# Performance work log

Measured on AMD Instinct MI355X. Metric: run time of the kernel, lower is better.

Reference implementation:

```python
import jax, jax.numpy as jnp
import numpy as np

N_NODES = 100000
IN_DIM = 128
HID = 128
N_EDGES = 1600000
N_PAIRS = 500000


def setup_inputs() -> dict:
    key = jax.random.key(0)
    ks = jax.random.split(key, 16)

    def lin(k, fan_out, fan_in):
        s = 1.0 / np.sqrt(fan_in)
        kw, kb = jax.random.split(k)
        W = jax.random.uniform(kw, (fan_out, fan_in), jnp.float32, -s, s)
        b = jax.random.uniform(kb, (fan_out,), jnp.float32, -s, s)
        return W, b

    x = jax.random.normal(ks[0], (N_NODES, IN_DIM), jnp.float32)
    edge_index = jax.random.randint(ks[1], (2, N_EDGES), 0, N_NODES, jnp.int64)
    edge_pairs = jax.random.randint(ks[2], (N_PAIRS, 2), 0, N_NODES, jnp.int64)

    # SAGEConv 1: lin_l (neighbor aggr, with bias), lin_r (root, no bias)
    W1l, b1l = lin(ks[3], HID, IN_DIM)
    W1r, _ = lin(ks[4], HID, IN_DIM)
    # SAGEConv 2
    W2l, b2l = lin(ks[5], HID, HID)
    W2r, _ = lin(ks[6], HID, HID)
    # MLP decoder
    Wm1, bm1 = lin(ks[7], HID, HID)
    Wm2, bm2 = lin(ks[8], HID // 2, HID)
    Wm3, bm3 = lin(ks[9], 1, HID // 2)

    return dict(x=x, edge_index=edge_index, edge_pairs=edge_pairs,
                W1l=W1l, b1l=b1l, W1r=W1r,
                W2l=W2l, b2l=b2l, W2r=W2r,
                Wm1=Wm1, bm1=bm1, Wm2=Wm2, bm2=bm2, Wm3=Wm3, bm3=bm3)


def _sage_conv(x, src, dst, Wl, bl, Wr):
    # mean aggregation of source-node features into destination nodes
    msg_sum = jax.ops.segment_sum(x[src], dst, num_segments=N_NODES)  # [N, D]
    cnt = jax.ops.segment_sum(jnp.ones((src.shape[0],), x.dtype), dst,
                              num_segments=N_NODES)
    aggr = msg_sum / jnp.maximum(cnt, 1.0)[:, None]
    return aggr @ Wl.T + bl + x @ Wr.T


def reference(x, edge_index, edge_pairs,
              W1l, b1l, W1r, W2l, b2l, W2r,
              Wm1, bm1, Wm2, bm2, Wm3, bm3):
    src, dst = edge_index[0], edge_index[1]
    # encode (eval mode: dropout = identity)
    h = jax.nn.relu(_sage_conv(x, src, dst, W1l, b1l, W1r))
    z = _sage_conv(h, src, dst, W2l, b2l, W2r)  # [N, HID]
    # decode
    hp = z[edge_pairs[:, 0]] * z[edge_pairs[:, 1]]  # [P, HID]
    hp = jax.nn.relu(hp @ Wm1.T + bm1)
    hp = jax.nn.relu(hp @ Wm2.T + bm2)
    return (hp @ Wm3.T + bm3).squeeze(-1)  # [P]
```

## Files before the change

kernel.cpp:

```cpp
#include <hip/hip_runtime.h>
#include <stdint.h>

typedef _Float16 half8 __attribute__((ext_vector_type(8)));
typedef float float4v __attribute__((ext_vector_type(4)));
typedef float floatx4 __attribute__((ext_vector_type(4)));
typedef int intx2 __attribute__((ext_vector_type(2)));

constexpr int kN = 100000;
constexpr int kE = 1600000;
constexpr int kP = 500000;
constexpr int NBS = (kN + 255) / 256;
constexpr int CT3 = kN / 16;
constexpr int DT2 = kP / 32;

__global__ void prep_kernel(
    const int* __restrict__ dst, int* __restrict__ deg, int* __restrict__ slot,
    const float* __restrict__ x, _Float16* __restrict__ xh,
    const float* __restrict__ W1l, const float* __restrict__ W1r,
    const float* __restrict__ W2l, const float* __restrict__ W2r,
    const float* __restrict__ Wm1, const float* __restrict__ Wm2,
    _Float16* __restrict__ CW1h, _Float16* __restrict__ CW1e,
    _Float16* __restrict__ CW2h, _Float16* __restrict__ CW2e,
    _Float16* __restrict__ M1h,  _Float16* __restrict__ M2h)
{
    const int b = blockIdx.x;
    if (b < 6250) {
        const int e = b * 256 + threadIdx.x;
        if (e < kE) slot[e] = atomicAdd(&deg[dst[e]], 1);
    } else if (b < 12500) {
        const int i = ((b - 6250) * 256 + threadIdx.x) * 8;
        if (i >= kN * 128) return;
        const floatx4 a = __builtin_nontemporal_load((const floatx4*)&x[i]);
        const floatx4 bb = __builtin_nontemporal_load((const floatx4*)&x[i + 4]);
        half8 v;
        v[0] = (_Float16)a[0]; v[1] = (_Float16)a[1]; v[2] = (_Float16)a[2]; v[3] = (_Float16)a[3];
        v[4] = (_Float16)bb[0]; v[5] = (_Float16)bb[1]; v[6] = (_Float16)bb[2]; v[7] = (_Float16)bb[3];
        *(half8*)&xh[i] = v;
    } else {
        const int i = (b - 12500) * 256 + threadIdx.x;
        if (i < 32768) {
            const int o = i >> 8, k = i & 255;
            const float w = (k < 128) ? W1l[o * 128 + k] : W1r[o * 128 + k - 128];
            const _Float16 h = (_Float16)w;
            CW1h[i] = h; CW1e[i] = (_Float16)(w - (float)h);
        } else if (i < 65536) {
            const int j = i - 32768;
            const int o = j >> 8, k = j & 255;
            const float w = (k < 128) ? W2l[o * 128 + k] : W2r[o * 128 + k - 128];
            const _Float16 h = (_Float16)w;
            CW2h[j] = h; CW2e[j] = (_Float16)(w - (float)h);
        } else if (i < 81920) {
            const int j = i - 65536;
            M1h[j] = (_Float16)Wm1[j];
        } else if (i < 90112) {
            const int j = i - 81920;
            M2h[j] = (_Float16)Wm2[j];
        }
    }
}

__global__ void scan_block_sums(const int* __restrict__ deg, int* __restrict__ bsum) {
    __shared__ int red[256];
    int t = threadIdx.x;
    int i = blockIdx.x * 256 + t;
    red[t] = (i < kN) ? deg[i] : 0;
    __syncthreads();
    for (int s = 128; s > 0; s >>= 1) {
        if (t < s) red[t] += red[t + s];
        __syncthreads();
    }
    if (t == 0) bsum[blockIdx.x] = red[0];
}

__global__ void scan_bsums(const int* __restrict__ bsum, int* __restrict__ boff) {
    __shared__ int sm[512];
    int t = threadIdx.x;
    int orig = (t < NBS) ? bsum[t] : 0;
    sm[t] = orig;
    __syncthreads();
    for (int d = 1; d < 512; d <<= 1) {
        int u = (t >= d) ? sm[t - d] : 0;
        __syncthreads();
        sm[t] += u;
        __syncthreads();
    }
    if (t < NBS) boff[t] = sm[t] - orig;
}

__global__ void scan_write(const int* __restrict__ deg, const int* __restrict__ boff,
                           int* __restrict__ row_start) {
    __shared__ int sm[256];
    int t = threadIdx.x;
    int i = blockIdx.x * 256 + t;
    int v = (i < kN) ? deg[i] : 0;
    sm[t] = v;
    __syncthreads();
    for (int d = 1; d < 256; d <<= 1) {
        int u = (t >= d) ? sm[t - d] : 0;
        __syncthreads();
        sm[t] += u;
        __syncthreads();
    }
    int excl = sm[t] - v + boff[blockIdx.x];
    if (i < kN) row_start[i] = excl;
    if (i == kN - 1) row_start[kN] = excl + v;
}

__global__ void fill2_kernel(const int* __restrict__ src, const int* __restrict__ dst,
                             const int* __restrict__ row_start,
                             const int* __restrict__ slot, int* __restrict__ srcs) {
    int e = blockIdx.x * blockDim.x + threadIdx.x;
    if (e < kE) srcs[row_start[dst[e]] + slot[e]] = src[e];
}

template <bool RELU>
__global__ __launch_bounds__(64, 4) void conv_mfma(
    const _Float16* __restrict__ xin,
    const int* __restrict__ row_start,
    const int* __restrict__ srcs,
    const _Float16* __restrict__ Wh,
    const _Float16* __restrict__ We,
    const float* __restrict__ bias,
    _Float16* __restrict__ out)
{
    __shared__ __align__(16) _Float16 stg[16 * 136];
    const int l = threadIdx.x & 63;
    const int p = l & 15;
    const int q = l >> 4;
    const int tile = blockIdx.x;
    const int c = p * 8;
    const int lbase = l & 48;

    int j0[4], j1[4];
#pragma unroll
    for (int s = 0; s < 4; s++) {
        const int n = tile * 16 + s * 4 + q;
        j0[s] = row_start[n];
        j1[s] = row_start[n + 1];
    }
    int idx16[4];
#pragma unroll
    for (int s = 0; s < 4; s++) {
        const int tA = j0[s] + p;
        const int v  = __builtin_nontemporal_load(&srcs[tA]);
        idx16[s] = (tA < j1[s]) ? v : 0;
    }

#pragma unroll
    for (int s = 0; s < 4; s++) {
        const int cnt = j1[s] - j0[s];
        float facc[8];
#pragma unroll
        for (int u = 0; u < 8; u++) facc[u] = 0.f;

        for (int jc = j0[s]; jc < j1[s]; jc += 16) {
            int myidx;
            if (jc == j0[s]) {
                myidx = idx16[s];
            } else {
                const int tB = jc + p;
                const int v  = __builtin_nontemporal_load(&srcs[tB]);
                myidx = (tB < j1[s]) ? v : 0;
            }
            half8 rows[16];
#pragma unroll
            for (int i = 0; i < 16; i++) {
                const int sidx = __shfl(myidx, lbase + i);
                rows[i] = *(const half8*)&xin[(size_t)sidx * 128 + c];
            }
            __builtin_amdgcn_sched_barrier(0);
            const int rem = j1[s] - jc;
#pragma unroll
            for (int i = 0; i < 16; i++) {
                if (i < rem) {
#pragma unroll
                    for (int u = 0; u < 8; u++) facc[u] += (float)rows[i][u];
                }
            }
        }
        const float inv = 1.0f / (float)(cnt > 1 ? cnt : 1);
        half8 hv;
#pragma unroll
        for (int u = 0; u < 8; u++) hv[u] = (_Float16)(facc[u] * inv);
        *(half8*)&stg[(s * 4 + q) * 136 + c] = hv;
    }

    half8 rt[4];
#pragma unroll
    for (int kt = 0; kt < 4; kt++)
        rt[kt] = *(const half8*)&xin[(size_t)(tile * 16 + p) * 128 + kt * 32 + q * 8];

    half8 am[4];
#pragma unroll
    for (int kt = 0; kt < 4; kt++)
        am[kt] = *(const half8*)&stg[p * 136 + kt * 32 + q * 8];

    float4v acc[8];
#pragma unroll
    for (int nt = 0; nt < 8; nt++) {
        const float b = bias[nt * 16 + p];
        acc[nt][0] = b; acc[nt][1] = b; acc[nt][2] = b; acc[nt][3] = b;
    }
#pragma unroll
    for (int kt = 0; kt < 8; kt++) {
        const half8 a = (kt < 4) ? am[kt] : rt[kt - 4];
#pragma unroll
        for (int nt = 0; nt < 8; nt++) {
            const int widx = (nt * 16 + p) * 256 + kt * 32 + q * 8;
            const half8 bh = *(const half8*)&Wh[widx];
            const half8 be = *(const half8*)&We[widx];
            acc[nt] = __builtin_amdgcn_mfma_f32_16x16x32_f16(a, bh, acc[nt], 0, 0, 0);
            acc[nt] = __builtin_amdgcn_mfma_f32_16x16x32_f16(a, be, acc[nt], 0, 0, 0);
        }
    }

#pragma unroll
    for (int nt = 0; nt < 8; nt++)
#pragma unroll
        for (int r = 0; r < 4; r++) {
            float v = acc[nt][r];
            if (RELU) v = fmaxf(v, 0.f);
            stg[(q * 4 + r) * 136 + nt * 16 + p] = (_Float16)v;
        }
    {
        const int row = l >> 2;
        const int c2  = (l & 3) * 8;
#pragma unroll
        for (int i = 0; i < 4; i++) {
            const half8 v = *(const half8*)&stg[row * 136 + i * 32 + c2];
            __builtin_nontemporal_store(v,
                (half8*)&out[(size_t)(tile * 16 + row) * 128 + i * 32 + c2]);
        }
    }
}

__global__ __launch_bounds__(64, 4) void decoder_mfma(
    const _Float16* __restrict__ z,
    const int* __restrict__ pairs,
    const _Float16* __restrict__ M1h, const float* __restrict__ bm1,
    const _Float16* __restrict__ M2h, const float* __restrict__ bm2,
    const float* __restrict__ Wm3, const float* __restrict__ bm3,
    float* __restrict__ outv)
{
    __shared__ __align__(16) _Float16 buf[32 * 136];
    const int l = threadIdx.x & 63;
    const int p = l & 15;
    const int q = l >> 4;
    const int tile = blockIdx.x;
    const int c = p * 8;

    intx2 ab[8];
#pragma unroll
    for (int it = 0; it < 8; it++)
        ab[it] = __builtin_nontemporal_load(
            (const intx2*)&pairs[(size_t)(tile * 32 + it * 4 + q) * 2]);
    half8 za[8], zb[8];
#pragma unroll
    for (int it = 0; it < 8; it++) {
        za[it] = *(const half8*)&z[(size_t)ab[it][0] * 128 + c];
        zb[it] = *(const half8*)&z[(size_t)ab[it][1] * 128 + c];
    }
    __builtin_amdgcn_sched_barrier(0);
#pragma unroll
    for (int it = 0; it < 8; it++)
        *(half8*)&buf[(it * 4 + q) * 136 + c] = za[it] * zb[it];

    half8 a1[2][4];
#pragma unroll
    for (int m = 0; m < 2; m++)
#pragma unroll
        for (int kt = 0; kt < 4; kt++)
            a1[m][kt] = *(const half8*)&buf[(m * 16 + p) * 136 + kt * 32 + q * 8];

    float4v acc1[2][8];
#pragma unroll
    for (int nt = 0; nt < 8; nt++) {
        const float b = bm1[nt * 16 + p];
#pragma unroll
        for (int m = 0; m < 2; m++) {
            acc1[m][nt][0] = b; acc1[m][nt][1] = b; acc1[m][nt][2] = b; acc1[m][nt][3] = b;
        }
    }
#pragma unroll
    for (int kt = 0; kt < 4; kt++)
#pragma unroll
        for (int nt = 0; nt < 8; nt++) {
            const half8 bh = *(const half8*)&M1h[(nt * 16 + p) * 128 + kt * 32 + q * 8];
            acc1[0][nt] = __builtin_amdgcn_mfma_f32_16x16x32_f16(a1[0][kt], bh, acc1[0][nt], 0, 0, 0);
            acc1[1][nt] = __builtin_amdgcn_mfma_f32_16x16x32_f16(a1[1][kt], bh, acc1[1][nt], 0, 0, 0);
        }

#pragma unroll
    for (int m = 0; m < 2; m++)
#pragma unroll
        for (int nt = 0; nt < 8; nt++)
#pragma unroll
            for (int r = 0; r < 4; r++)
                buf[(m * 16 + q * 4 + r) * 136 + nt * 16 + p] =
                    (_Float16)fmaxf(acc1[m][nt][r], 0.f);

    half8 a2[2][4];
#pragma unroll
    for (int m = 0; m < 2; m++)
#pragma unroll
        for (int kt = 0; kt < 4; kt++)
            a2[m][kt] = *(const half8*)&buf[(m * 16 + p) * 136 + kt * 32 + q * 8];

    float4v acc2[2][4];
#pragma unroll
    for (int nt = 0; nt < 4; nt++) {
        const float b = bm2[nt * 16 + p];
#pragma unroll
        for (int m = 0; m < 2; m++) {
            acc2[m][nt][0] = b; acc2[m][nt][1] = b; acc2[m][nt][2] = b; acc2[m][nt][3] = b;
        }
    }
#pragma unroll
    for (int kt = 0; kt < 4; kt++)
#pragma unroll
        for (int nt = 0; nt < 4; nt++) {
            const half8 bh = *(const half8*)&M2h[(nt * 16 + p) * 128 + kt * 32 + q * 8];
            acc2[0][nt] = __builtin_amdgcn_mfma_f32_16x16x32_f16(a2[0][kt], bh, acc2[0][nt], 0, 0, 0);
            acc2[1][nt] = __builtin_amdgcn_mfma_f32_16x16x32_f16(a2[1][kt], bh, acc2[1][nt], 0, 0, 0);
        }

    float wm3v[4];
#pragma unroll
    for (int nt = 0; nt < 4; nt++) wm3v[nt] = Wm3[nt * 16 + p];
    const float b3 = bm3[0];
#pragma unroll
    for (int m = 0; m < 2; m++) {
        float part[4];
#pragma unroll
        for (int r = 0; r < 4; r++) part[r] = 0.f;
#pragma unroll
        for (int nt = 0; nt < 4; nt++)
#pragma unroll
            for (int r = 0; r < 4; r++)
                part[r] += fmaxf(acc2[m][nt][r], 0.f) * wm3v[nt];
#pragma unroll
        for (int s = 1; s <= 8; s <<= 1)
#pragma unroll
            for (int r = 0; r < 4; r++) part[r] += __shfl_xor(part[r], s);
        if (p == 0) {
            floatx4 o;
            o[0] = part[0] + b3; o[1] = part[1] + b3;
            o[2] = part[2] + b3; o[3] = part[3] + b3;
            __builtin_nontemporal_store(o, (floatx4*)&outv[tile * 32 + m * 16 + q * 4]);
        }
    }
}

extern "C" void kernel_launch(void* const* d_in, const int* in_sizes, int n_in,
                              void* d_out, int out_size, void* d_ws, size_t ws_size,
                              hipStream_t stream) {
    const float* x   = (const float*)d_in[0];
    const int*   src = (const int*)d_in[1];
    const int*   dst = src + kE;
    const int*   ep  = (const int*)d_in[2];
    const float* W1l = (const float*)d_in[3];
    const float* b1l = (const float*)d_in[4];
    const float* W1r = (const float*)d_in[5];
    const float* W2l = (const float*)d_in[6];
    const float* b2l = (const float*)d_in[7];
    const float* W2r = (const float*)d_in[8];
    const float* Wm1 = (const float*)d_in[9];
    const float* bm1 = (const float*)d_in[10];
    const float* Wm2 = (const float*)d_in[11];
    const float* bm2 = (const float*)d_in[12];
    const float* Wm3 = (const float*)d_in[13];
    const float* bm3 = (const float*)d_in[14];
    float* outv = (float*)d_out;

    char* ws = (char*)d_ws;
    size_t off = 0;
    auto alloc = [&](size_t bytes) -> void* {
        void* p = ws + off;
        off += bytes;
        off = (off + 255) & ~(size_t)255;
        return p;
    };
    int*      deg       = (int*)alloc((size_t)kN * 4);
    int*      row_start = (int*)alloc((size_t)(kN + 1) * 4);
    int*      slot      = (int*)alloc((size_t)kE * 4);
    int*      bsum      = (int*)alloc(512 * 4);
    int*      boff      = (int*)alloc(512 * 4);
    int*      srcs      = (int*)alloc((size_t)(kE + 64) * 4);
    _Float16* xh        = (_Float16*)alloc((size_t)kN * 128 * 2);
    _Float16* hh        = (_Float16*)alloc((size_t)kN * 128 * 2);
    _Float16* zh        = (_Float16*)alloc((size_t)kN * 128 * 2);
    _Float16* CW1h      = (_Float16*)alloc(128 * 256 * 2);
    _Float16* CW1e      = (_Float16*)alloc(128 * 256 * 2);
    _Float16* CW2h      = (_Float16*)alloc(128 * 256 * 2);
    _Float16* CW2e      = (_Float16*)alloc(128 * 256 * 2);
    _Float16* M1h       = (_Float16*)alloc(128 * 128 * 2);
    _Float16* M2h       = (_Float16*)alloc(64 * 128 * 2);

    hipMemsetAsync(deg, 0, (size_t)kN * sizeof(int), stream);
    prep_kernel<<<12852, 256, 0, stream>>>(dst, deg, slot, x, xh,
                                           W1l, W1r, W2l, W2r, Wm1, Wm2,
                                           CW1h, CW1e, CW2h, CW2e, M1h, M2h);
    scan_block_sums<<<NBS, 256, 0, stream>>>(deg, bsum);
    scan_bsums<<<1, 512, 0, stream>>>(bsum, boff);
    scan_write<<<NBS, 256, 0, stream>>>(deg, boff, row_start);
    fill2_kernel<<<(kE + 255) / 256, 256, 0, stream>>>(src, dst, row_start, slot, srcs);

    conv_mfma<true><<<CT3, 64, 0, stream>>>(xh, row_start, srcs, CW1h, CW1e, b1l, hh);
    conv_mfma<false><<<CT3, 64, 0, stream>>>(hh, row_start, srcs, CW2h, CW2e, b2l, zh);

    decoder_mfma<<<DT2, 64, 0, stream>>>(
        zh, ep, M1h, bm1, M2h, bm2, Wm3, bm3, outv);
}
```

Measured before the change: 606.5 us.

## Replace per-edge slot array with atomic cursors and fold block-sum scan into scan_write

The degree-count atomics no longer return and store a per-edge slot, which removes a 1.6M-int write and its later read. The fill step now places each edge with an atomicAdd on a per-node cursor initialized from row_start. The separate single-block scan of block sums is removed: each scan_write block sums the preceding block totals itself, saving one launch. The trade is a second pass of contended atomics in fill and a nondeterministic neighbor order within each row, which can change floating-point summation order.

```diff
diff --git a/kernel.cpp b/kernel.cpp
--- a/kernel.cpp
+++ b/kernel.cpp
@@ -14,7 +14,7 @@
 constexpr int DT2 = kP / 32;
 
 __global__ void prep_kernel(
-    const int* __restrict__ dst, int* __restrict__ deg, int* __restrict__ slot,
+    const int* __restrict__ dst, int* __restrict__ deg,
     const float* __restrict__ x, _Float16* __restrict__ xh,
     const float* __restrict__ W1l, const float* __restrict__ W1r,
     const float* __restrict__ W2l, const float* __restrict__ W2r,
@@ -26,7 +26,7 @@
     const int b = blockIdx.x;
     if (b < 6250) {
         const int e = b * 256 + threadIdx.x;
-        if (e < kE) slot[e] = atomicAdd(&deg[dst[e]], 1);
+        if (e < kE) atomicAdd(&deg[dst[e]], 1);
     } else if (b < 12500) {
         const int i = ((b - 6250) * 256 + threadIdx.x) * 8;
         if (i >= kN * 128) return;
@@ -72,27 +72,22 @@
     if (t == 0) bsum[blockIdx.x] = red[0];
 }
 
-__global__ void scan_bsums(const int* __restrict__ bsum, int* __restrict__ boff) {
-    __shared__ int sm[512];
-    int t = threadIdx.x;
-    int orig = (t < NBS) ? bsum[t] : 0;
-    sm[t] = orig;
+__global__ void scan_write(const int* __restrict__ deg, const int* __restrict__ bsum,
+                           int* __restrict__ row_start, int* __restrict__ cursor) {
+    __shared__ int sm[256];
+    const int t = threadIdx.x;
+    int part = 0;
+    for (int j = t; j < blockIdx.x; j += 256) part += bsum[j];
+    sm[t] = part;
     __syncthreads();
-    for (int d = 1; d < 512; d <<= 1) {
-        int u = (t >= d) ? sm[t - d] : 0;
+    for (int s = 128; s > 0; s >>= 1) {
+        if (t < s) sm[t] += sm[t + s];
         __syncthreads();
-        sm[t] += u;
-        __syncthreads();
-    }
-    if (t < NBS) boff[t] = sm[t] - orig;
-}
-
-__global__ void scan_write(const int* __restrict__ deg, const int* __restrict__ boff,
-                           int* __restrict__ row_start) {
-    __shared__ int sm[256];
-    int t = threadIdx.x;
-    int i = blockIdx.x * 256 + t;
-    int v = (i < kN) ? deg[i] : 0;
+    }
+    const int boff = sm[0];
+    __syncthreads();
+    const int i = blockIdx.x * 256 + t;
+    const int v = (i < kN) ? deg[i] : 0;
     sm[t] = v;
     __syncthreads();
     for (int d = 1; d < 256; d <<= 1) {
@@ -101,16 +96,18 @@
         sm[t] += u;
         __syncthreads();
     }
-    int excl = sm[t] - v + boff[blockIdx.x];
-    if (i < kN) row_start[i] = excl;
+    const int excl = sm[t] - v + boff;
+    if (i < kN) { row_start[i] = excl; cursor[i] = excl; }
     if (i == kN - 1) row_start[kN] = excl + v;
 }
 
 __global__ void fill2_kernel(const int* __restrict__ src, const int* __restrict__ dst,
-                             const int* __restrict__ row_start,
-                             const int* __restrict__ slot, int* __restrict__ srcs) {
+                             int* __restrict__ cursor, int* __restrict__ srcs) {
     int e = blockIdx.x * blockDim.x + threadIdx.x;
-    if (e < kE) srcs[row_start[dst[e]] + slot[e]] = src[e];
+    if (e < kE) {
+        const int pos = atomicAdd(&cursor[dst[e]], 1);
+        srcs[pos] = src[e];
+    }
 }
 
 template <bool RELU>
@@ -382,9 +379,8 @@
     };
     int*      deg       = (int*)alloc((size_t)kN * 4);
     int*      row_start = (int*)alloc((size_t)(kN + 1) * 4);
-    int*      slot      = (int*)alloc((size_t)kE * 4);
+    int*      cursor    = (int*)alloc((size_t)kN * 4);
     int*      bsum      = (int*)alloc(512 * 4);
-    int*      boff      = (int*)alloc(512 * 4);
     int*      srcs      = (int*)alloc((size_t)(kE + 64) * 4);
     _Float16* xh        = (_Float16*)alloc((size_t)kN * 128 * 2);
     _Float16* hh        = (_Float16*)alloc((size_t)kN * 128 * 2);
@@ -397,13 +393,12 @@
     _Float16* M2h       = (_Float16*)alloc(64 * 128 * 2);
 
     hipMemsetAsync(deg, 0, (size_t)kN * sizeof(int), stream);
-    prep_kernel<<<12852, 256, 0, stream>>>(dst, deg, slot, x, xh,
+    prep_kernel<<<12852, 256, 0, stream>>>(dst, deg, x, xh,
                                            W1l, W1r, W2l, W2r, Wm1, Wm2,
                                            CW1h, CW1e, CW2h, CW2e, M1h, M2h);
     scan_block_sums<<<NBS, 256, 0, stream>>>(deg, bsum);
-    scan_bsums<<<1, 512, 0, stream>>>(bsum, boff);
-    scan_write<<<NBS, 256, 0, stream>>>(deg, boff, row_start);
-    fill2_kernel<<<(kE + 255) / 256, 256, 0, stream>>>(src, dst, row_start, slot, srcs);
+    scan_write<<<NBS, 256, 0, stream>>>(deg, bsum, row_start, cursor);
+    fill2_kernel<<<(kE + 255) / 256, 256, 0, stream>>>(src, dst, cursor, srcs);
 
     conv_mfma<true><<<CT3, 64, 0, stream>>>(xh, row_start, srcs, CW1h, CW1e, b1l, hh);
     conv_mfma<false><<<CT3, 64, 0, stream>>>(hh, row_start, srcs, CW2h, CW2e, b2l, zh);
```

Result: slower. 694.4 us (+14.5%).
